# Optimization experiments

Measured on AMD Instinct MI355X. Metric: run time of the kernel, lower is better.

Reference implementation:

```python
import jax, jax.numpy as jnp
import numpy as np

N_NODES = 100000
N_EDGES = 640000
IN_CH, HID_CH, OUT_CH = 256, 128, 64


def setup_inputs() -> dict:
    key = jax.random.key(0)
    ks = jax.random.split(key, 6)
    x = jax.random.normal(ks[0], (N_NODES, IN_CH), dtype=jnp.float32)
    edge_index = jax.random.randint(ks[1], (2, N_EDGES), 0, N_NODES, dtype=jnp.int32)
    # Glorot-style init for GCNConv weights
    W1 = jax.random.normal(ks[2], (IN_CH, HID_CH), dtype=jnp.float32) * (1.0 / np.sqrt(IN_CH))
    W_mu = jax.random.normal(ks[3], (HID_CH, OUT_CH), dtype=jnp.float32) * (1.0 / np.sqrt(HID_CH))
    W_logvar = jax.random.normal(ks[4], (HID_CH, OUT_CH), dtype=jnp.float32) * (1.0 / np.sqrt(HID_CH))
    return {
        "x": x,
        "edge_index": edge_index,
        "W1": W1,
        "b1": jnp.zeros((HID_CH,), jnp.float32),
        "W_mu": W_mu,
        "b_mu": jnp.zeros((OUT_CH,), jnp.float32),
        "W_logvar": W_logvar,
        "b_logvar": jnp.zeros((OUT_CH,), jnp.float32),
    }


def reference(x, edge_index, W1, b1, W_mu, b_mu, W_logvar, b_logvar):
    N = x.shape[0]
    # PyG GCNConv default: add self-loops, symmetric normalization D^-1/2 A_hat D^-1/2
    loops = jnp.arange(N, dtype=edge_index.dtype)
    src = jnp.concatenate([edge_index[0], loops])  # [E+N]
    dst = jnp.concatenate([edge_index[1], loops])  # [E+N]
    deg = jax.ops.segment_sum(jnp.ones_like(src, dtype=x.dtype), dst, num_segments=N)
    dinv = jax.lax.rsqrt(deg)  # deg >= 1 due to self-loops
    norm = dinv[src] * dinv[dst]  # [E+N]

    def gcn_conv(h, W, b):
        h = h @ W                                   # [N, d_out]
        msg = h[src] * norm[:, None]                # gather + scale  [E+N, d_out]
        out = jax.ops.segment_sum(msg, dst, num_segments=N)  # scatter-add
        return out + b

    h = jax.nn.relu(gcn_conv(x, W1, b1))
    mu = gcn_conv(h, W_mu, b_mu)
    logvar = gcn_conv(h, W_logvar, b_logvar)
    return (mu, logvar)
```

## Files before the change

kernel.cpp:

```cpp
#include <hip/hip_runtime.h>
#include <hip/hip_bf16.h>

#define N_NODES 100000
#define E_EDGES 640000

typedef __attribute__((ext_vector_type(8))) short short8;
typedef __attribute__((ext_vector_type(4))) float float4v;

__device__ __forceinline__ float bf2f(unsigned int u16) {
    union { unsigned int i; float f; } c; c.i = u16 << 16; return c.f;
}
__device__ __forceinline__ unsigned short f2bf(float f) {
    union { float f; unsigned int i; } c; c.f = f;
    unsigned int x = c.i;
    unsigned int r = (x + 0x7fffu + ((x >> 16) & 1u)) >> 16;
    return (unsigned short)r;
}

#define ASYNC16(g, l)                                                          \
    __builtin_amdgcn_global_load_lds(                                          \
        (const __attribute__((address_space(1))) void*)(g),                    \
        (__attribute__((address_space(3))) void*)(l), 16, 0, 0)

#define WS_HIST    0
#define WS_CURSOR  524288
#define WS_OFFS    1048576
#define WS_DINV    1572864
#define WS_BSUMS   2097152
#define WS_EIDX    2621440
#define WS_WP1     7864320
#define WS_WP2     7929856
#define WS_H0      7962624
#define WS_H       33562624

__global__ __launch_bounds__(256) void k_hist(const int* __restrict__ dst, int* __restrict__ hist) {
    int e = blockIdx.x * 256 + threadIdx.x;
    if (e < E_EDGES) atomicAdd(&hist[dst[e]], 1);
}

__global__ __launch_bounds__(256) void k_scan1(const int* __restrict__ hist,
                                               int* __restrict__ offs,
                                               int* __restrict__ bsums,
                                               float* __restrict__ dinv) {
    __shared__ int sd[256];
    int t = threadIdx.x;
    int base = blockIdx.x * 1024 + t * 4;
    int v[4];
#pragma unroll
    for (int j = 0; j < 4; ++j) v[j] = (base + j < N_NODES) ? hist[base + j] : 0;
#pragma unroll
    for (int j = 0; j < 4; ++j)
        if (base + j < N_NODES) dinv[base + j] = rsqrtf((float)(v[j] + 1));
    int s = v[0] + v[1] + v[2] + v[3];
    sd[t] = s;
    __syncthreads();
    for (int d = 1; d < 256; d <<= 1) {
        int x = (t >= d) ? sd[t - d] : 0;
        __syncthreads();
        sd[t] += x;
        __syncthreads();
    }
    int excl = sd[t] - s;
    if (t == 255) bsums[blockIdx.x] = sd[255];
    int run = excl;
#pragma unroll
    for (int j = 0; j < 4; ++j) {
        if (base + j < N_NODES) offs[base + j] = run;
        run += v[j];
    }
}

__global__ __launch_bounds__(128) void k_scan2(int* __restrict__ bsums, int nb) {
    __shared__ int sd[128];
    int t = threadIdx.x;
    int v = (t < nb) ? bsums[t] : 0;
    sd[t] = v;
    __syncthreads();
    for (int d = 1; d < 128; d <<= 1) {
        int x = (t >= d) ? sd[t - d] : 0;
        __syncthreads();
        sd[t] += x;
        __syncthreads();
    }
    if (t < nb) bsums[t] = sd[t] - v;
}

__global__ __launch_bounds__(256) void k_scan3(int* __restrict__ offs, const int* __restrict__ bsums) {
    int i = blockIdx.x * 256 + threadIdx.x;
    if (i < N_NODES) offs[i] += bsums[i >> 10];
}

__global__ __launch_bounds__(256) void k_fill(const int* __restrict__ src, const int* __restrict__ dst,
                                              const int* __restrict__ offs, int* __restrict__ cursor,
                                              const float* __restrict__ dinv,
                                              int2* __restrict__ eidx) {
    int e = blockIdx.x * 256 + threadIdx.x;
    if (e < E_EDGES) {
        int s = src[e], d = dst[e];
        int p = offs[d] + atomicAdd(&cursor[d], 1);
        int2 v;
        v.x = s;
        v.y = __float_as_int(dinv[s] * dinv[d]);
        eidx[p] = v;
    }
}

__global__ __launch_bounds__(256) void k_pack(const float* __restrict__ W1,
                                              const float* __restrict__ Wmu,
                                              const float* __restrict__ Wlv,
                                              unsigned short* __restrict__ Wp1,
                                              unsigned short* __restrict__ Wp2) {
    int i = blockIdx.x * 256 + threadIdx.x;
    if (i < 256 * 128) {
        int k = i >> 7, n = i & 127;
        Wp1[n * 256 + k] = f2bf(W1[i]);
    }
    if (i < 128 * 128) {
        int k = i >> 7, n = i & 127;
        float w = (n < 64) ? Wmu[k * 64 + n] : Wlv[k * 64 + (n - 64)];
        Wp2[n * 128 + k] = f2bf(w);
    }
}

__global__ __launch_bounds__(256) void k_mgemm1(const float* __restrict__ A,
                                                const unsigned short* __restrict__ Bpack,
                                                unsigned short* __restrict__ out) {
    __shared__ float As[128 * 32];
    __shared__ unsigned short Bs[128 * 40];
    int tid = threadIdx.x;
    int row0 = blockIdx.x * 128;
    int wave = tid >> 6, lane = tid & 63;
    int c = lane & 15, q = lane >> 4;
    int wrow = (wave >> 1) * 64, wcol = (wave & 1) * 64;

    float4v acc[4][4];
#pragma unroll
    for (int i = 0; i < 4; ++i)
#pragma unroll
        for (int j = 0; j < 4; ++j) acc[i][j] = (float4v){0.f, 0.f, 0.f, 0.f};

    int srow = tid >> 1;
    int shalf = (tid & 1) * 16;

    for (int k0 = 0; k0 < 256; k0 += 32) {
        const unsigned short* bsrc = Bpack + (size_t)srow * 256 + k0 + shalf;
        short8 b0 = *(const short8*)(bsrc);
        short8 b1 = *(const short8*)(bsrc + 8);
#pragma unroll
        for (int t = 0; t < 4; ++t) {
            int S = (t * 4 + wave) * 64 + lane;
            int row = S >> 3, j = S & 7;
            int kq = j ^ (row & 7);
            const float* g = A + (size_t)(row0 + row) * 256 + k0 + kq * 4;
            float* ldst = As + (t * 4 + wave) * 256;
            if (row0 + row < N_NODES) ASYNC16(g, ldst);
        }
        *(short8*)(&Bs[srow * 40 + shalf])     = b0;
        *(short8*)(&Bs[srow * 40 + shalf + 8]) = b1;
        __syncthreads();

        short8 af[4], bfr[4];
#pragma unroll
        for (int mt = 0; mt < 4; ++mt) {
            int r = wrow + mt * 16 + c;
            int j0 = (q * 2) ^ (r & 7);
            float4v fa = *(const float4v*)(&As[r * 32 + j0 * 4]);
            float4v fb = *(const float4v*)(&As[r * 32 + (j0 ^ 1) * 4]);
            short8 s;
#pragma unroll
            for (int jj = 0; jj < 4; ++jj) s[jj]     = (short)f2bf(fa[jj]);
#pragma unroll
            for (int jj = 0; jj < 4; ++jj) s[4 + jj] = (short)f2bf(fb[jj]);
            af[mt] = s;
        }
#pragma unroll
        for (int nt = 0; nt < 4; ++nt)
            bfr[nt] = *(const short8*)(&Bs[(wcol + nt * 16 + c) * 40 + q * 8]);
#pragma unroll
        for (int mt = 0; mt < 4; ++mt)
#pragma unroll
            for (int nt = 0; nt < 4; ++nt)
                acc[mt][nt] = __builtin_amdgcn_mfma_f32_16x16x32_bf16(af[mt], bfr[nt], acc[mt][nt], 0, 0, 0);
        __syncthreads();
    }

#pragma unroll
    for (int mt = 0; mt < 4; ++mt) {
#pragma unroll
        for (int i = 0; i < 4; ++i) {
            int row = row0 + wrow + mt * 16 + q * 4 + i;
            if (row >= N_NODES) continue;
#pragma unroll
            for (int nt = 0; nt < 4; ++nt) {
                int cc = wcol + nt * 16 + c;
                out[(size_t)row * 128 + cc] = f2bf(acc[mt][nt][i]);
            }
        }
    }
}

__global__ __launch_bounds__(256) void k_mgemm2(const unsigned short* __restrict__ A,
                                                const unsigned short* __restrict__ Bpack,
                                                const float* __restrict__ bias0,
                                                const float* __restrict__ bias1,
                                                float* __restrict__ out) {
    constexpr int LDT = 40;
    __shared__ unsigned short As[128 * LDT];
    __shared__ unsigned short Bs[128 * LDT];
    int tid = threadIdx.x;
    int row0 = blockIdx.x * 128;
    int wave = tid >> 6, lane = tid & 63;
    int c = lane & 15, q = lane >> 4;
    int wrow = (wave >> 1) * 64, wcol = (wave & 1) * 64;

    float4v acc[4][4];
#pragma unroll
    for (int i = 0; i < 4; ++i)
#pragma unroll
        for (int j = 0; j < 4; ++j) acc[i][j] = (float4v){0.f, 0.f, 0.f, 0.f};

    int srow = tid >> 1, shalf = (tid & 1) * 16;
    const short8 zed = {0, 0, 0, 0, 0, 0, 0, 0};

    for (int k0 = 0; k0 < 128; k0 += 32) {
        const unsigned short* bsrc = Bpack + (size_t)srow * 128 + k0 + shalf;
        short8 b0 = *(const short8*)(bsrc);
        short8 b1 = *(const short8*)(bsrc + 8);
        int grow = row0 + srow;
        short8 a0 = zed, a1 = zed;
        if (grow < N_NODES) {
            const unsigned short* asrc = A + (size_t)grow * 128 + k0 + shalf;
            a0 = *(const short8*)(asrc);
            a1 = *(const short8*)(asrc + 8);
        }
        *(short8*)(&Bs[srow * LDT + shalf])     = b0;
        *(short8*)(&Bs[srow * LDT + shalf + 8]) = b1;
        *(short8*)(&As[srow * LDT + shalf])     = a0;
        *(short8*)(&As[srow * LDT + shalf + 8]) = a1;
        __syncthreads();

        short8 af[4], bfr[4];
#pragma unroll
        for (int mt = 0; mt < 4; ++mt)
            af[mt] = *(const short8*)(&As[(wrow + mt * 16 + c) * LDT + q * 8]);
#pragma unroll
        for (int nt = 0; nt < 4; ++nt)
            bfr[nt] = *(const short8*)(&Bs[(wcol + nt * 16 + c) * LDT + q * 8]);
#pragma unroll
        for (int mt = 0; mt < 4; ++mt)
#pragma unroll
            for (int nt = 0; nt < 4; ++nt)
                acc[mt][nt] = __builtin_amdgcn_mfma_f32_16x16x32_bf16(af[mt], bfr[nt], acc[mt][nt], 0, 0, 0);
        __syncthreads();
    }

#pragma unroll
    for (int mt = 0; mt < 4; ++mt) {
#pragma unroll
        for (int i = 0; i < 4; ++i) {
            int row = row0 + wrow + mt * 16 + q * 4 + i;
            if (row >= N_NODES) continue;
#pragma unroll
            for (int nt = 0; nt < 4; ++nt) {
                int cc = wcol + nt * 16 + c;
                float v = acc[mt][nt][i];
                if (cc < 64) out[(size_t)row * 64 + cc] = v + bias0[cc];
                else out[(size_t)N_NODES * 64 + (size_t)row * 64 + (cc - 64)] = v + bias1[cc - 64];
            }
        }
    }
}

template <int BIAS_RELU>
__global__ __launch_bounds__(256) void k_agg(const unsigned int* __restrict__ in,
                                             unsigned int* __restrict__ out,
                                             const float* __restrict__ dinv,
                                             const int2* __restrict__ eidx,
                                             const int* __restrict__ offs,
                                             const int* __restrict__ cnt,
                                             const float* __restrict__ bias) {
    int wid = (blockIdx.x * 256 + threadIdx.x) >> 6;
    if (wid >= N_NODES) return;
    int l = threadIdx.x & 63;
    float di = dinv[wid];
    unsigned int u = in[(size_t)wid * 64 + l];
    float sc = di * di;
    float ax = sc * bf2f(u & 0xffffu);
    float ay = sc * bf2f(u >> 16);
    if (BIAS_RELU) { ax += bias[2 * l]; ay += bias[2 * l + 1]; }
    int start = offs[wid];
    int n = cnt[wid];

    for (int base = 0; base < n; base += 64) {
        int m = min(n - base, 64);
        int sreg = 0; float wreg = 0.f;
        if (l < m) {
            int2 ev = eidx[start + base + l];
            sreg = ev.x;
            wreg = __int_as_float(ev.y);
        }
        int e = 0;
        for (; e + 4 <= m; e += 4) {
            int s0 = __shfl(sreg, e),     s1 = __shfl(sreg, e + 1);
            int s2 = __shfl(sreg, e + 2), s3 = __shfl(sreg, e + 3);
            float w0 = __shfl(wreg, e),     w1 = __shfl(wreg, e + 1);
            float w2 = __shfl(wreg, e + 2), w3 = __shfl(wreg, e + 3);
            unsigned int u0 = in[(size_t)s0 * 64 + l];
            unsigned int u1 = in[(size_t)s1 * 64 + l];
            unsigned int u2 = in[(size_t)s2 * 64 + l];
            unsigned int u3 = in[(size_t)s3 * 64 + l];
            ax += w0 * bf2f(u0 & 0xffffu); ay += w0 * bf2f(u0 >> 16);
            ax += w1 * bf2f(u1 & 0xffffu); ay += w1 * bf2f(u1 >> 16);
            ax += w2 * bf2f(u2 & 0xffffu); ay += w2 * bf2f(u2 >> 16);
            ax += w3 * bf2f(u3 & 0xffffu); ay += w3 * bf2f(u3 >> 16);
        }
        for (; e < m; ++e) {
            int s0 = __shfl(sreg, e);
            float w0 = __shfl(wreg, e);
            unsigned int u0 = in[(size_t)s0 * 64 + l];
            ax += w0 * bf2f(u0 & 0xffffu); ay += w0 * bf2f(u0 >> 16);
        }
    }
    if (BIAS_RELU) { ax = fmaxf(ax, 0.f); ay = fmaxf(ay, 0.f); }
    out[(size_t)wid * 64 + l] = (unsigned int)f2bf(ax) | ((unsigned int)f2bf(ay) << 16);
}

extern "C" void kernel_launch(void* const* d_in, const int* in_sizes, int n_in,
                              void* d_out, int out_size, void* d_ws, size_t ws_size,
                              hipStream_t stream) {
    const float* x    = (const float*)d_in[0];
    const int*   ei   = (const int*)d_in[1];
    const float* W1   = (const float*)d_in[2];
    const float* b1   = (const float*)d_in[3];
    const float* Wmu  = (const float*)d_in[4];
    const float* bmu  = (const float*)d_in[5];
    const float* Wlv  = (const float*)d_in[6];
    const float* blv  = (const float*)d_in[7];
    float* outp = (float*)d_out;

    const int* src = ei;
    const int* dst = ei + E_EDGES;

    char* ws = (char*)d_ws;
    int*            hist   = (int*)(ws + WS_HIST);
    int*            cursor = (int*)(ws + WS_CURSOR);
    int*            offs   = (int*)(ws + WS_OFFS);
    float*          dinv   = (float*)(ws + WS_DINV);
    int*            bsums  = (int*)(ws + WS_BSUMS);
    int2*           eidx   = (int2*)(ws + WS_EIDX);
    unsigned short* Wp1    = (unsigned short*)(ws + WS_WP1);
    unsigned short* Wp2    = (unsigned short*)(ws + WS_WP2);
    unsigned short* h0     = (unsigned short*)(ws + WS_H0);
    unsigned short* h      = (unsigned short*)(ws + WS_H);

    const int NB_N = (N_NODES + 255) / 256;
    const int NB_E = (E_EDGES + 255) / 256;
    const int NB_S = (N_NODES + 1023) / 1024;
    const int NB_G = (N_NODES + 127) / 128;

    hipMemsetAsync(ws + WS_HIST, 0, 1048576, stream);
    k_hist<<<NB_E, 256, 0, stream>>>(dst, hist);
    k_scan1<<<NB_S, 256, 0, stream>>>(hist, offs, bsums, dinv);
    k_scan2<<<1, 128, 0, stream>>>(bsums, NB_S);
    k_scan3<<<NB_N, 256, 0, stream>>>(offs, bsums);
    k_fill<<<NB_E, 256, 0, stream>>>(src, dst, offs, cursor, dinv, eidx);
    k_pack<<<128, 256, 0, stream>>>(W1, Wmu, Wlv, Wp1, Wp2);

    k_mgemm1<<<NB_G, 256, 0, stream>>>(x, Wp1, h0);
    k_agg<1><<<(N_NODES * 64 + 255) / 256, 256, 0, stream>>>(
        (const unsigned int*)h0, (unsigned int*)h, dinv, eidx, offs, hist, b1);

    k_agg<0><<<(N_NODES * 64 + 255) / 256, 256, 0, stream>>>(
        (const unsigned int*)h, (unsigned int*)h0, dinv, eidx, offs, hist, nullptr);
    k_mgemm2<<<NB_G, 256, 0, stream>>>(h0, Wp2, bmu, blv, outp);
}
```

Measured before the change: 361.2 us.

## Persistent strip GEMMs with LDS-resident weights; fuse hist/pack and drop scan3

Both dense GEMMs become persistent kernels that load the whole packed bf16 weight matrix into LDS once per block. Each wave then computes 16-row strips across all 128 output columns, reading A directly from global memory with no per-k-tile syncs. The weight packing is merged into the histogram kernel, and the scan3 pass is removed by adding block sums at use sites in fill and aggregation. This cuts launches and barriers, at the cost of larger LDS use and A loads that are no longer staged through LDS.

```diff
diff --git a/kernel.cpp b/kernel.cpp
--- a/kernel.cpp
+++ b/kernel.cpp
@@ -3,6 +3,7 @@
 
 #define N_NODES 100000
 #define E_EDGES 640000
+#define NSTRIP  6250
 
 typedef __attribute__((ext_vector_type(8))) short short8;
 typedef __attribute__((ext_vector_type(4))) float float4v;
@@ -33,9 +34,29 @@
 #define WS_H0      7962624
 #define WS_H       33562624
 
-__global__ __launch_bounds__(256) void k_hist(const int* __restrict__ dst, int* __restrict__ hist) {
-    int e = blockIdx.x * 256 + threadIdx.x;
-    if (e < E_EDGES) atomicAdd(&hist[dst[e]], 1);
+#define NB_E 2500
+__global__ __launch_bounds__(256) void k_hist_pack(const int* __restrict__ dst, int* __restrict__ hist,
+                                                   const float* __restrict__ W1,
+                                                   const float* __restrict__ Wmu,
+                                                   const float* __restrict__ Wlv,
+                                                   unsigned short* __restrict__ Wp1,
+                                                   unsigned short* __restrict__ Wp2) {
+    int b = blockIdx.x;
+    if (b < NB_E) {
+        int e = b * 256 + threadIdx.x;
+        if (e < E_EDGES) atomicAdd(&hist[dst[e]], 1);
+    } else {
+        int i = (b - NB_E) * 256 + threadIdx.x;
+        if (i < 256 * 128) {
+            int k = i >> 7, n = i & 127;
+            Wp1[n * 256 + k] = f2bf(W1[i]);
+        }
+        if (i < 128 * 128) {
+            int k = i >> 7, n = i & 127;
+            float w = (n < 64) ? Wmu[k * 64 + n] : Wlv[k * 64 + (n - 64)];
+            Wp2[n * 128 + k] = f2bf(w);
+        }
+    }
 }
 
 __global__ __launch_bounds__(256) void k_scan1(const int* __restrict__ hist,
@@ -85,19 +106,15 @@
     if (t < nb) bsums[t] = sd[t] - v;
 }
 
-__global__ __launch_bounds__(256) void k_scan3(int* __restrict__ offs, const int* __restrict__ bsums) {
-    int i = blockIdx.x * 256 + threadIdx.x;
-    if (i < N_NODES) offs[i] += bsums[i >> 10];
-}
-
 __global__ __launch_bounds__(256) void k_fill(const int* __restrict__ src, const int* __restrict__ dst,
-                                              const int* __restrict__ offs, int* __restrict__ cursor,
+                                              const int* __restrict__ offs, const int* __restrict__ bsums,
+                                              int* __restrict__ cursor,
                                               const float* __restrict__ dinv,
                                               int2* __restrict__ eidx) {
     int e = blockIdx.x * 256 + threadIdx.x;
     if (e < E_EDGES) {
         int s = src[e], d = dst[e];
-        int p = offs[d] + atomicAdd(&cursor[d], 1);
+        int p = offs[d] + bsums[d >> 10] + atomicAdd(&cursor[d], 1);
         int2 v;
         v.x = s;
         v.y = __float_as_int(dinv[s] * dinv[d]);
@@ -105,168 +122,106 @@
     }
 }
 
-__global__ __launch_bounds__(256) void k_pack(const float* __restrict__ W1,
-                                              const float* __restrict__ Wmu,
-                                              const float* __restrict__ Wlv,
-                                              unsigned short* __restrict__ Wp1,
-                                              unsigned short* __restrict__ Wp2) {
-    int i = blockIdx.x * 256 + threadIdx.x;
-    if (i < 256 * 128) {
-        int k = i >> 7, n = i & 127;
-        Wp1[n * 256 + k] = f2bf(W1[i]);
-    }
-    if (i < 128 * 128) {
-        int k = i >> 7, n = i & 127;
-        float w = (n < 64) ? Wmu[k * 64 + n] : Wlv[k * 64 + (n - 64)];
-        Wp2[n * 128 + k] = f2bf(w);
-    }
-}
-
-__global__ __launch_bounds__(256) void k_mgemm1(const float* __restrict__ A,
-                                                const unsigned short* __restrict__ Bpack,
-                                                unsigned short* __restrict__ out) {
-    __shared__ float As[128 * 32];
-    __shared__ unsigned short Bs[128 * 40];
+__global__ __launch_bounds__(512, 4) void k_mgemm1(const float* __restrict__ A,
+                                                   const unsigned short* __restrict__ Bpack,
+                                                   unsigned short* __restrict__ out) {
+    __shared__ unsigned short Bs[128 * 256];
     int tid = threadIdx.x;
-    int row0 = blockIdx.x * 128;
     int wave = tid >> 6, lane = tid & 63;
     int c = lane & 15, q = lane >> 4;
-    int wrow = (wave >> 1) * 64, wcol = (wave & 1) * 64;
-
-    float4v acc[4][4];
-#pragma unroll
-    for (int i = 0; i < 4; ++i)
-#pragma unroll
-        for (int j = 0; j < 4; ++j) acc[i][j] = (float4v){0.f, 0.f, 0.f, 0.f};
-
-    int srow = tid >> 1;
-    int shalf = (tid & 1) * 16;
-
-    for (int k0 = 0; k0 < 256; k0 += 32) {
-        const unsigned short* bsrc = Bpack + (size_t)srow * 256 + k0 + shalf;
-        short8 b0 = *(const short8*)(bsrc);
-        short8 b1 = *(const short8*)(bsrc + 8);
-#pragma unroll
-        for (int t = 0; t < 4; ++t) {
-            int S = (t * 4 + wave) * 64 + lane;
-            int row = S >> 3, j = S & 7;
-            int kq = j ^ (row & 7);
-            const float* g = A + (size_t)(row0 + row) * 256 + k0 + kq * 4;
-            float* ldst = As + (t * 4 + wave) * 256;
-            if (row0 + row < N_NODES) ASYNC16(g, ldst);
-        }
-        *(short8*)(&Bs[srow * 40 + shalf])     = b0;
-        *(short8*)(&Bs[srow * 40 + shalf + 8]) = b1;
-        __syncthreads();
-
-        short8 af[4], bfr[4];
-#pragma unroll
-        for (int mt = 0; mt < 4; ++mt) {
-            int r = wrow + mt * 16 + c;
-            int j0 = (q * 2) ^ (r & 7);
-            float4v fa = *(const float4v*)(&As[r * 32 + j0 * 4]);
-            float4v fb = *(const float4v*)(&As[r * 32 + (j0 ^ 1) * 4]);
-            short8 s;
-#pragma unroll
-            for (int jj = 0; jj < 4; ++jj) s[jj]     = (short)f2bf(fa[jj]);
-#pragma unroll
-            for (int jj = 0; jj < 4; ++jj) s[4 + jj] = (short)f2bf(fb[jj]);
-            af[mt] = s;
-        }
-#pragma unroll
-        for (int nt = 0; nt < 4; ++nt)
-            bfr[nt] = *(const short8*)(&Bs[(wcol + nt * 16 + c) * 40 + q * 8]);
-#pragma unroll
-        for (int mt = 0; mt < 4; ++mt)
-#pragma unroll
-            for (int nt = 0; nt < 4; ++nt)
-                acc[mt][nt] = __builtin_amdgcn_mfma_f32_16x16x32_bf16(af[mt], bfr[nt], acc[mt][nt], 0, 0, 0);
-        __syncthreads();
-    }
-
-#pragma unroll
-    for (int mt = 0; mt < 4; ++mt) {
-#pragma unroll
-        for (int i = 0; i < 4; ++i) {
-            int row = row0 + wrow + mt * 16 + q * 4 + i;
-            if (row >= N_NODES) continue;
-#pragma unroll
-            for (int nt = 0; nt < 4; ++nt) {
-                int cc = wcol + nt * 16 + c;
-                out[(size_t)row * 128 + cc] = f2bf(acc[mt][nt][i]);
+
+#pragma unroll
+    for (int i = 0; i < 8; ++i) {
+        int Gb = (i * 8 + wave) * 64;
+        int G = Gb + lane;
+        int n = G >> 5, gp = G & 31;
+        int gl = gp ^ (n & 7);
+        ASYNC16(Bpack + (size_t)n * 256 + gl * 8, Bs + (size_t)Gb * 8);
+    }
+    __syncthreads();
+
+    int w = blockIdx.x * 8 + wave;
+    int sw = c & 7;
+    for (int s = w; s < NSTRIP; s += 4096) {
+        const float* ap = A + (size_t)(s * 16 + c) * 256 + q * 8;
+        float4v acc[8];
+#pragma unroll
+        for (int nt = 0; nt < 8; ++nt) acc[nt] = (float4v){0.f, 0.f, 0.f, 0.f};
+#pragma unroll
+        for (int kc = 0; kc < 8; ++kc) {
+            float4v fa = *(const float4v*)(ap + kc * 32);
+            float4v fb = *(const float4v*)(ap + kc * 32 + 4);
+            short8 af;
+#pragma unroll
+            for (int jj = 0; jj < 4; ++jj) {
+                af[jj]     = (short)f2bf(fa[jj]);
+                af[4 + jj] = (short)f2bf(fb[jj]);
             }
-        }
-    }
-}
-
-__global__ __launch_bounds__(256) void k_mgemm2(const unsigned short* __restrict__ A,
-                                                const unsigned short* __restrict__ Bpack,
-                                                const float* __restrict__ bias0,
-                                                const float* __restrict__ bias1,
-                                                float* __restrict__ out) {
-    constexpr int LDT = 40;
-    __shared__ unsigned short As[128 * LDT];
-    __shared__ unsigned short Bs[128 * LDT];
+            int pg = (kc * 4 + q) ^ sw;
+#pragma unroll
+            for (int nt = 0; nt < 8; ++nt) {
+                short8 bfr = *(const short8*)(&Bs[((nt * 16 + c) << 8) + (pg << 3)]);
+                acc[nt] = __builtin_amdgcn_mfma_f32_16x16x32_bf16(af, bfr, acc[nt], 0, 0, 0);
+            }
+        }
+        int orow = s * 16 + q * 4;
+#pragma unroll
+        for (int nt = 0; nt < 8; ++nt) {
+            int col = nt * 16 + c;
+#pragma unroll
+            for (int i = 0; i < 4; ++i)
+                out[(size_t)(orow + i) * 128 + col] = f2bf(acc[nt][i]);
+        }
+    }
+}
+
+__global__ __launch_bounds__(512, 4) void k_mgemm2(const unsigned short* __restrict__ A,
+                                                   const unsigned short* __restrict__ Bpack,
+                                                   const float* __restrict__ bias0,
+                                                   const float* __restrict__ bias1,
+                                                   float* __restrict__ out) {
+    __shared__ unsigned short Bs[128 * 128];
     int tid = threadIdx.x;
-    int row0 = blockIdx.x * 128;
     int wave = tid >> 6, lane = tid & 63;
     int c = lane & 15, q = lane >> 4;
-    int wrow = (wave >> 1) * 64, wcol = (wave & 1) * 64;
-
-    float4v acc[4][4];
-#pragma unroll
-    for (int i = 0; i < 4; ++i)
-#pragma unroll
-        for (int j = 0; j < 4; ++j) acc[i][j] = (float4v){0.f, 0.f, 0.f, 0.f};
-
-    int srow = tid >> 1, shalf = (tid & 1) * 16;
-    const short8 zed = {0, 0, 0, 0, 0, 0, 0, 0};
-
-    for (int k0 = 0; k0 < 128; k0 += 32) {
-        const unsigned short* bsrc = Bpack + (size_t)srow * 128 + k0 + shalf;
-        short8 b0 = *(const short8*)(bsrc);
-        short8 b1 = *(const short8*)(bsrc + 8);
-        int grow = row0 + srow;
-        short8 a0 = zed, a1 = zed;
-        if (grow < N_NODES) {
-            const unsigned short* asrc = A + (size_t)grow * 128 + k0 + shalf;
-            a0 = *(const short8*)(asrc);
-            a1 = *(const short8*)(asrc + 8);
-        }
-        *(short8*)(&Bs[srow * LDT + shalf])     = b0;
-        *(short8*)(&Bs[srow * LDT + shalf + 8]) = b1;
-        *(short8*)(&As[srow * LDT + shalf])     = a0;
-        *(short8*)(&As[srow * LDT + shalf + 8]) = a1;
-        __syncthreads();
-
-        short8 af[4], bfr[4];
-#pragma unroll
-        for (int mt = 0; mt < 4; ++mt)
-            af[mt] = *(const short8*)(&As[(wrow + mt * 16 + c) * LDT + q * 8]);
-#pragma unroll
-        for (int nt = 0; nt < 4; ++nt)
-            bfr[nt] = *(const short8*)(&Bs[(wcol + nt * 16 + c) * LDT + q * 8]);
-#pragma unroll
-        for (int mt = 0; mt < 4; ++mt)
-#pragma unroll
-            for (int nt = 0; nt < 4; ++nt)
-                acc[mt][nt] = __builtin_amdgcn_mfma_f32_16x16x32_bf16(af[mt], bfr[nt], acc[mt][nt], 0, 0, 0);
-        __syncthreads();
-    }
-
-#pragma unroll
-    for (int mt = 0; mt < 4; ++mt) {
-#pragma unroll
-        for (int i = 0; i < 4; ++i) {
-            int row = row0 + wrow + mt * 16 + q * 4 + i;
-            if (row >= N_NODES) continue;
-#pragma unroll
-            for (int nt = 0; nt < 4; ++nt) {
-                int cc = wcol + nt * 16 + c;
-                float v = acc[mt][nt][i];
-                if (cc < 64) out[(size_t)row * 64 + cc] = v + bias0[cc];
-                else out[(size_t)N_NODES * 64 + (size_t)row * 64 + (cc - 64)] = v + bias1[cc - 64];
+
+#pragma unroll
+    for (int i = 0; i < 4; ++i) {
+        int Gb = (i * 8 + wave) * 64;
+        int G = Gb + lane;
+        int n = G >> 4, gp = G & 15;
+        int gl = gp ^ (n & 7);
+        ASYNC16(Bpack + (size_t)n * 128 + gl * 8, Bs + (size_t)Gb * 8);
+    }
+    __syncthreads();
+
+    int w = blockIdx.x * 8 + wave;
+    int sw = c & 7;
+    for (int s = w; s < NSTRIP; s += 4096) {
+        const unsigned short* ap = A + (size_t)(s * 16 + c) * 128 + q * 8;
+        float4v acc[8];
+#pragma unroll
+        for (int nt = 0; nt < 8; ++nt) acc[nt] = (float4v){0.f, 0.f, 0.f, 0.f};
+#pragma unroll
+        for (int kc = 0; kc < 4; ++kc) {
+            short8 af = *(const short8*)(ap + kc * 32);
+            int pg = (kc * 4 + q) ^ sw;
+#pragma unroll
+            for (int nt = 0; nt < 8; ++nt) {
+                short8 bfr = *(const short8*)(&Bs[((nt * 16 + c) << 7) + (pg << 3)]);
+                acc[nt] = __builtin_amdgcn_mfma_f32_16x16x32_bf16(af, bfr, acc[nt], 0, 0, 0);
             }
+        }
+        int orow = s * 16 + q * 4;
+#pragma unroll
+        for (int nt = 0; nt < 8; ++nt) {
+            int col = nt * 16 + c;
+            float bv = (col < 64) ? bias0[col] : bias1[col - 64];
+            float* dst = (col < 64) ? (out + (size_t)orow * 64 + col)
+                                    : (out + (size_t)N_NODES * 64 + (size_t)orow * 64 + (col - 64));
+#pragma unroll
+            for (int i = 0; i < 4; ++i)
+                dst[(size_t)i * 64] = acc[nt][i] + bv;
         }
     }
 }
@@ -277,6 +232,7 @@
                                              const float* __restrict__ dinv,
                                              const int2* __restrict__ eidx,
                                              const int* __restrict__ offs,
+                                             const int* __restrict__ bsums,
                                              const int* __restrict__ cnt,
                                              const float* __restrict__ bias) {
     int wid = (blockIdx.x * 256 + threadIdx.x) >> 6;
@@ -288,7 +244,7 @@
     float ax = sc * bf2f(u & 0xffffu);
     float ay = sc * bf2f(u >> 16);
     if (BIAS_RELU) { ax += bias[2 * l]; ay += bias[2 * l + 1]; }
-    int start = offs[wid];
+    int start = offs[wid] + bsums[wid >> 10];
     int n = cnt[wid];
 
     for (int base = 0; base < n; base += 64) {
@@ -353,24 +309,19 @@
     unsigned short* h0     = (unsigned short*)(ws + WS_H0);
     unsigned short* h      = (unsigned short*)(ws + WS_H);
 
-    const int NB_N = (N_NODES + 255) / 256;
-    const int NB_E = (E_EDGES + 255) / 256;
     const int NB_S = (N_NODES + 1023) / 1024;
-    const int NB_G = (N_NODES + 127) / 128;
 
     hipMemsetAsync(ws + WS_HIST, 0, 1048576, stream);
-    k_hist<<<NB_E, 256, 0, stream>>>(dst, hist);
+    k_hist_pack<<<NB_E + 128, 256, 0, stream>>>(dst, hist, W1, Wmu, Wlv, Wp1, Wp2);
     k_scan1<<<NB_S, 256, 0, stream>>>(hist, offs, bsums, dinv);
     k_scan2<<<1, 128, 0, stream>>>(bsums, NB_S);
-    k_scan3<<<NB_N, 256, 0, stream>>>(offs, bsums);
-    k_fill<<<NB_E, 256, 0, stream>>>(src, dst, offs, cursor, dinv, eidx);
-    k_pack<<<128, 256, 0, stream>>>(W1, Wmu, Wlv, Wp1, Wp2);
-
-    k_mgemm1<<<NB_G, 256, 0, stream>>>(x, Wp1, h0);
+    k_fill<<<NB_E, 256, 0, stream>>>(src, dst, offs, bsums, cursor, dinv, eidx);
+
+    k_mgemm1<<<512, 512, 0, stream>>>(x, Wp1, h0);
     k_agg<1><<<(N_NODES * 64 + 255) / 256, 256, 0, stream>>>(
-        (const unsigned int*)h0, (unsigned int*)h, dinv, eidx, offs, hist, b1);
+        (const unsigned int*)h0, (unsigned int*)h, dinv, eidx, offs, bsums, hist, b1);
 
     k_agg<0><<<(N_NODES * 64 + 255) / 256, 256, 0, stream>>>(
-        (const unsigned int*)h, (unsigned int*)h0, dinv, eidx, offs, hist, nullptr);
-    k_mgemm2<<<NB_G, 256, 0, stream>>>(h0, Wp2, bmu, blv, outp);
-}
+        (const unsigned int*)h, (unsigned int*)h0, dinv, eidx, offs, bsums, hist, nullptr);
+    k_mgemm2<<<512, 512, 0, stream>>>(h0, Wp2, bmu, blv, outp);
+}
```

Result: slower. 485.3 us (+34.4%).

## Merge hist with weight pack, drop scan3 kernel, halve GEMM row tiles

Applied to the files above, without the earlier changes.

Weight packing is folded into the histogram kernel as extra blocks. The scan3 fixup kernel is removed by having fill and the aggregation kernels add the per-block sum when they read offsets. Both MFMA GEMMs shrink from 128-row to 64-row tiles with a launch-bounds occupancy hint, which doubles the block count and cuts register and LDS use per block. These cut launch overhead and raise occupancy, at the price of an extra load per offset read and less reuse of the B tile per block.

```diff
diff --git a/kernel.cpp b/kernel.cpp
--- a/kernel.cpp
+++ b/kernel.cpp
@@ -33,9 +33,29 @@
 #define WS_H0      7962624
 #define WS_H       33562624
 
-__global__ __launch_bounds__(256) void k_hist(const int* __restrict__ dst, int* __restrict__ hist) {
-    int e = blockIdx.x * 256 + threadIdx.x;
-    if (e < E_EDGES) atomicAdd(&hist[dst[e]], 1);
+#define NB_E 2500
+__global__ __launch_bounds__(256) void k_hist_pack(const int* __restrict__ dst, int* __restrict__ hist,
+                                                   const float* __restrict__ W1,
+                                                   const float* __restrict__ Wmu,
+                                                   const float* __restrict__ Wlv,
+                                                   unsigned short* __restrict__ Wp1,
+                                                   unsigned short* __restrict__ Wp2) {
+    int b = blockIdx.x;
+    if (b < NB_E) {
+        int e = b * 256 + threadIdx.x;
+        if (e < E_EDGES) atomicAdd(&hist[dst[e]], 1);
+    } else {
+        int i = (b - NB_E) * 256 + threadIdx.x;
+        if (i < 256 * 128) {
+            int k = i >> 7, n = i & 127;
+            Wp1[n * 256 + k] = f2bf(W1[i]);
+        }
+        if (i < 128 * 128) {
+            int k = i >> 7, n = i & 127;
+            float w = (n < 64) ? Wmu[k * 64 + n] : Wlv[k * 64 + (n - 64)];
+            Wp2[n * 128 + k] = f2bf(w);
+        }
+    }
 }
 
 __global__ __launch_bounds__(256) void k_scan1(const int* __restrict__ hist,
@@ -85,19 +105,15 @@
     if (t < nb) bsums[t] = sd[t] - v;
 }
 
-__global__ __launch_bounds__(256) void k_scan3(int* __restrict__ offs, const int* __restrict__ bsums) {
-    int i = blockIdx.x * 256 + threadIdx.x;
-    if (i < N_NODES) offs[i] += bsums[i >> 10];
-}
-
 __global__ __launch_bounds__(256) void k_fill(const int* __restrict__ src, const int* __restrict__ dst,
-                                              const int* __restrict__ offs, int* __restrict__ cursor,
+                                              const int* __restrict__ offs, const int* __restrict__ bsums,
+                                              int* __restrict__ cursor,
                                               const float* __restrict__ dinv,
                                               int2* __restrict__ eidx) {
     int e = blockIdx.x * 256 + threadIdx.x;
     if (e < E_EDGES) {
         int s = src[e], d = dst[e];
-        int p = offs[d] + atomicAdd(&cursor[d], 1);
+        int p = offs[d] + bsums[d >> 10] + atomicAdd(&cursor[d], 1);
         int2 v;
         v.x = s;
         v.y = __float_as_int(dinv[s] * dinv[d]);
@@ -105,37 +121,20 @@
     }
 }
 
-__global__ __launch_bounds__(256) void k_pack(const float* __restrict__ W1,
-                                              const float* __restrict__ Wmu,
-                                              const float* __restrict__ Wlv,
-                                              unsigned short* __restrict__ Wp1,
-                                              unsigned short* __restrict__ Wp2) {
-    int i = blockIdx.x * 256 + threadIdx.x;
-    if (i < 256 * 128) {
-        int k = i >> 7, n = i & 127;
-        Wp1[n * 256 + k] = f2bf(W1[i]);
-    }
-    if (i < 128 * 128) {
-        int k = i >> 7, n = i & 127;
-        float w = (n < 64) ? Wmu[k * 64 + n] : Wlv[k * 64 + (n - 64)];
-        Wp2[n * 128 + k] = f2bf(w);
-    }
-}
-
-__global__ __launch_bounds__(256) void k_mgemm1(const float* __restrict__ A,
-                                                const unsigned short* __restrict__ Bpack,
-                                                unsigned short* __restrict__ out) {
-    __shared__ float As[128 * 32];
+__global__ __launch_bounds__(256, 6) void k_mgemm1(const float* __restrict__ A,
+                                                   const unsigned short* __restrict__ Bpack,
+                                                   unsigned short* __restrict__ out) {
+    __shared__ float As[64 * 32];
     __shared__ unsigned short Bs[128 * 40];
     int tid = threadIdx.x;
-    int row0 = blockIdx.x * 128;
+    int row0 = blockIdx.x * 64;
     int wave = tid >> 6, lane = tid & 63;
     int c = lane & 15, q = lane >> 4;
-    int wrow = (wave >> 1) * 64, wcol = (wave & 1) * 64;
-
-    float4v acc[4][4];
-#pragma unroll
-    for (int i = 0; i < 4; ++i)
+    int wrow = (wave >> 1) * 32, wcol = (wave & 1) * 64;
+
+    float4v acc[2][4];
+#pragma unroll
+    for (int i = 0; i < 2; ++i)
 #pragma unroll
         for (int j = 0; j < 4; ++j) acc[i][j] = (float4v){0.f, 0.f, 0.f, 0.f};
 
@@ -147,21 +146,22 @@
         short8 b0 = *(const short8*)(bsrc);
         short8 b1 = *(const short8*)(bsrc + 8);
 #pragma unroll
-        for (int t = 0; t < 4; ++t) {
-            int S = (t * 4 + wave) * 64 + lane;
+        for (int t = 0; t < 2; ++t) {
+            int grp = t * 4 + wave;
+            int S = grp * 64 + lane;
             int row = S >> 3, j = S & 7;
             int kq = j ^ (row & 7);
             const float* g = A + (size_t)(row0 + row) * 256 + k0 + kq * 4;
-            float* ldst = As + (t * 4 + wave) * 256;
+            float* ldst = As + grp * 256;
             if (row0 + row < N_NODES) ASYNC16(g, ldst);
         }
         *(short8*)(&Bs[srow * 40 + shalf])     = b0;
         *(short8*)(&Bs[srow * 40 + shalf + 8]) = b1;
         __syncthreads();
 
-        short8 af[4], bfr[4];
-#pragma unroll
-        for (int mt = 0; mt < 4; ++mt) {
+        short8 af[2], bfr[4];
+#pragma unroll
+        for (int mt = 0; mt < 2; ++mt) {
             int r = wrow + mt * 16 + c;
             int j0 = (q * 2) ^ (r & 7);
             float4v fa = *(const float4v*)(&As[r * 32 + j0 * 4]);
@@ -177,7 +177,7 @@
         for (int nt = 0; nt < 4; ++nt)
             bfr[nt] = *(const short8*)(&Bs[(wcol + nt * 16 + c) * 40 + q * 8]);
 #pragma unroll
-        for (int mt = 0; mt < 4; ++mt)
+        for (int mt = 0; mt < 2; ++mt)
 #pragma unroll
             for (int nt = 0; nt < 4; ++nt)
                 acc[mt][nt] = __builtin_amdgcn_mfma_f32_16x16x32_bf16(af[mt], bfr[nt], acc[mt][nt], 0, 0, 0);
@@ -185,7 +185,7 @@
     }
 
 #pragma unroll
-    for (int mt = 0; mt < 4; ++mt) {
+    for (int mt = 0; mt < 2; ++mt) {
 #pragma unroll
         for (int i = 0; i < 4; ++i) {
             int row = row0 + wrow + mt * 16 + q * 4 + i;
@@ -199,55 +199,52 @@
     }
 }
 
-__global__ __launch_bounds__(256) void k_mgemm2(const unsigned short* __restrict__ A,
-                                                const unsigned short* __restrict__ Bpack,
-                                                const float* __restrict__ bias0,
-                                                const float* __restrict__ bias1,
-                                                float* __restrict__ out) {
+__global__ __launch_bounds__(256, 6) void k_mgemm2(const unsigned short* __restrict__ A,
+                                                   const unsigned short* __restrict__ Bpack,
+                                                   const float* __restrict__ bias0,
+                                                   const float* __restrict__ bias1,
+                                                   float* __restrict__ out) {
     constexpr int LDT = 40;
-    __shared__ unsigned short As[128 * LDT];
+    __shared__ unsigned short As[64 * LDT];
     __shared__ unsigned short Bs[128 * LDT];
     int tid = threadIdx.x;
-    int row0 = blockIdx.x * 128;
+    int row0 = blockIdx.x * 64;
     int wave = tid >> 6, lane = tid & 63;
     int c = lane & 15, q = lane >> 4;
-    int wrow = (wave >> 1) * 64, wcol = (wave & 1) * 64;
-
-    float4v acc[4][4];
-#pragma unroll
-    for (int i = 0; i < 4; ++i)
+    int wrow = (wave >> 1) * 32, wcol = (wave & 1) * 64;
+
+    float4v acc[2][4];
+#pragma unroll
+    for (int i = 0; i < 2; ++i)
 #pragma unroll
         for (int j = 0; j < 4; ++j) acc[i][j] = (float4v){0.f, 0.f, 0.f, 0.f};
 
     int srow = tid >> 1, shalf = (tid & 1) * 16;
+    int arow = tid >> 2, aoff = (tid & 3) * 8;
     const short8 zed = {0, 0, 0, 0, 0, 0, 0, 0};
 
     for (int k0 = 0; k0 < 128; k0 += 32) {
         const unsigned short* bsrc = Bpack + (size_t)srow * 128 + k0 + shalf;
         short8 b0 = *(const short8*)(bsrc);
         short8 b1 = *(const short8*)(bsrc + 8);
-        int grow = row0 + srow;
-        short8 a0 = zed, a1 = zed;
-        if (grow < N_NODES) {
-            const unsigned short* asrc = A + (size_t)grow * 128 + k0 + shalf;
-            a0 = *(const short8*)(asrc);
-            a1 = *(const short8*)(asrc + 8);
-        }
+        int grow = row0 + arow;
+        short8 a0 = zed;
+        if (grow < N_NODES)
+            a0 = *(const short8*)(A + (size_t)grow * 128 + k0 + aoff);
         *(short8*)(&Bs[srow * LDT + shalf])     = b0;
         *(short8*)(&Bs[srow * LDT + shalf + 8]) = b1;
-        *(short8*)(&As[srow * LDT + shalf])     = a0;
-        *(short8*)(&As[srow * LDT + shalf + 8]) = a1;
-        __syncthreads();
-
-        short8 af[4], bfr[4];
-#pragma unroll
-        for (int mt = 0; mt < 4; ++mt)
+        *(short8*)(&As[arow * LDT + aoff])      = a0;
+        __syncthreads();
+
+        short8 af[2], bfr[4];
+#pragma unroll
+        for (int mt = 0; mt < 2; ++mt)
             af[mt] = *(const short8*)(&As[(wrow + mt * 16 + c) * LDT + q * 8]);
 #pragma unroll
         for (int nt = 0; nt < 4; ++nt)
             bfr[nt] = *(const short8*)(&Bs[(wcol + nt * 16 + c) * LDT + q * 8]);
 #pragma unroll
-        for (int mt = 0; mt < 4; ++mt)
+        for (int mt = 0; mt < 2; ++mt)
 #pragma unroll
             for (int nt = 0; nt < 4; ++nt)
                 acc[mt][nt] = __builtin_amdgcn_mfma_f32_16x16x32_bf16(af[mt], bfr[nt], acc[mt][nt], 0, 0, 0);
@@ -255,7 +252,7 @@
     }
 
 #pragma unroll
-    for (int mt = 0; mt < 4; ++mt) {
+    for (int mt = 0; mt < 2; ++mt) {
 #pragma unroll
         for (int i = 0; i < 4; ++i) {
             int row = row0 + wrow + mt * 16 + q * 4 + i;
@@ -277,6 +274,7 @@
                                              const float* __restrict__ dinv,
                                              const int2* __restrict__ eidx,
                                              const int* __restrict__ offs,
+                                             const int* __restrict__ bsums,
                                              const int* __restrict__ cnt,
                                              const float* __restrict__ bias) {
     int wid = (blockIdx.x * 256 + threadIdx.x) >> 6;
@@ -288,7 +286,7 @@
     float ax = sc * bf2f(u & 0xffffu);
     float ay = sc * bf2f(u >> 16);
     if (BIAS_RELU) { ax += bias[2 * l]; ay += bias[2 * l + 1]; }
-    int start = offs[wid];
+    int start = offs[wid] + bsums[wid >> 10];
     int n = cnt[wid];
 
     for (int base = 0; base < n; base += 64) {
@@ -353,24 +351,20 @@
     unsigned short* h0     = (unsigned short*)(ws + WS_H0);
     unsigned short* h      = (unsigned short*)(ws + WS_H);
 
-    const int NB_N = (N_NODES + 255) / 256;
-    const int NB_E = (E_EDGES + 255) / 256;
     const int NB_S = (N_NODES + 1023) / 1024;
-    const int NB_G = (N_NODES + 127) / 128;
+    const int NB_G = (N_NODES + 63) / 64;
 
     hipMemsetAsync(ws + WS_HIST, 0, 1048576, stream);
-    k_hist<<<NB_E, 256, 0, stream>>>(dst, hist);
+    k_hist_pack<<<NB_E + 128, 256, 0, stream>>>(dst, hist, W1, Wmu, Wlv, Wp1, Wp2);
     k_scan1<<<NB_S, 256, 0, stream>>>(hist, offs, bsums, dinv);
     k_scan2<<<1, 128, 0, stream>>>(bsums, NB_S);
-    k_scan3<<<NB_N, 256, 0, stream>>>(offs, bsums);
-    k_fill<<<NB_E, 256, 0, stream>>>(src, dst, offs, cursor, dinv, eidx);
-    k_pack<<<128, 256, 0, stream>>>(W1, Wmu, Wlv, Wp1, Wp2);
+    k_fill<<<NB_E, 256, 0, stream>>>(src, dst, offs, bsums, cursor, dinv, eidx);
 
     k_mgemm1<<<NB_G, 256, 0, stream>>>(x, Wp1, h0);
     k_agg<1><<<(N_NODES * 64 + 255) / 256, 256, 0, stream>>>(
-        (const unsigned int*)h0, (unsigned int*)h, dinv, eidx, offs, hist, b1);
+        (const unsigned int*)h0, (unsigned int*)h, dinv, eidx, offs, bsums, hist, b1);
 
     k_agg<0><<<(N_NODES * 64 + 255) / 256, 256, 0, stream>>>(
-        (const unsigned int*)h, (unsigned int*)h0, dinv, eidx, offs, hist, nullptr);
+        (const unsigned int*)h, (unsigned int*)h0, dinv, eidx, offs, bsums, hist, nullptr);
     k_mgemm2<<<NB_G, 256, 0, stream>>>(h0, Wp2, bmu, blv, outp);
 }
```

After: 352.8 us. 2.3% less time.
